# Kernel optimization log

Measured on AMD Instinct MI355X. Metric: run time of the kernel, lower is better.

Reference implementation:

```python
import jax, jax.numpy as jnp
import numpy as np

N_NODES = 100000
N_EDGES = 1250000
N_GRAPHS = 1024
NUM_SHAPES = 16
NUM_COLORS = 16
NUM_CLASSES = 10


def setup_inputs() -> dict:
    key = jax.random.key(0)
    ks = jax.random.split(key, 16)
    x_tokens = jax.random.randint(ks[0], (N_NODES, 2), 0, NUM_SHAPES, dtype=jnp.int64) if jax.config.jax_enable_x64 else jax.random.randint(ks[0], (N_NODES, 2), 0, NUM_SHAPES, dtype=jnp.int32)
    edge_index = jax.random.randint(ks[1], (2, N_EDGES), 0, N_NODES, dtype=jnp.int32)
    batch = jnp.sort(jax.random.randint(ks[2], (N_NODES,), 0, N_GRAPHS, dtype=jnp.int32))
    def glorot(k, shape, fan_in):
        return jax.random.normal(k, shape, jnp.float32) / jnp.sqrt(jnp.float32(fan_in))
    return {
        "x_tokens": x_tokens,
        "edge_index": edge_index,
        "batch": batch,
        "shape_emb": jax.random.normal(ks[3], (NUM_SHAPES, 8), jnp.float32),
        "color_emb": jax.random.normal(ks[4], (NUM_COLORS, 8), jnp.float32),
        "lin_w": glorot(ks[5], (32, 16), 16),
        "lin_b": jnp.zeros((32,), jnp.float32),
        "conv1_wrel": glorot(ks[6], (64, 32), 32),
        "conv1_brel": jnp.zeros((64,), jnp.float32),
        "conv1_wroot": glorot(ks[7], (64, 32), 32),
        "conv2_wrel": glorot(ks[8], (64, 64), 64),
        "conv2_brel": jnp.zeros((64,), jnp.float32),
        "conv2_wroot": glorot(ks[9], (64, 64), 64),
        "cls_w": glorot(ks[10], (NUM_CLASSES, 64), 64),
        "cls_b": jnp.zeros((NUM_CLASSES,), jnp.float32),
    }


def _graph_conv(x, src, dst, w_rel, b_rel, w_root):
    # PyG GraphConv (aggr='add'): out_i = W_rel @ sum_{j->i} x_j + b_rel + W_root @ x_i
    agg = jax.ops.segment_sum(x[src], dst, num_segments=x.shape[0])  # [N, d_in]
    return agg @ w_rel.T + b_rel + x @ w_root.T


def reference(x_tokens, edge_index, batch, shape_emb, color_emb, lin_w, lin_b,
              conv1_wrel, conv1_brel, conv1_wroot,
              conv2_wrel, conv2_brel, conv2_wroot, cls_w, cls_b):
    src, dst = edge_index[0], edge_index[1]
    # embed shape/color tokens and concat -> [N, 16]
    x = jnp.concatenate([shape_emb[x_tokens[:, 0]], color_emb[x_tokens[:, 1]]], axis=1)
    x = jax.nn.relu(x @ lin_w.T + lin_b)                      # [N, 32]
    x = jax.nn.relu(_graph_conv(x, src, dst, conv1_wrel, conv1_brel, conv1_wroot))  # [N, 64]
    x = jax.nn.relu(_graph_conv(x, src, dst, conv2_wrel, conv2_brel, conv2_wroot))  # [N, 64]
    # global mean pool over graphs
    sums = jax.ops.segment_sum(x, batch, num_segments=N_GRAPHS)           # [G, 64]
    counts = jax.ops.segment_sum(jnp.ones((x.shape[0],), x.dtype), batch, num_segments=N_GRAPHS)
    pooled = sums / jnp.maximum(counts, 1.0)[:, None]
    return pooled @ cls_w.T + cls_b                            # [G, num_classes]
```

## Files before the change

kernel.cpp:

```cpp
#include <hip/hip_runtime.h>

#define N_NODES  100000
#define N_EDGES  1250000
#define N_GRAPHS 1024
#define NB       ((N_NODES + 127) >> 7)
#define NB2      (N_NODES / 16)
#define NBLK_F   500
#define EPB      (N_EDGES / NBLK_F)
#define EMB_BLKS ((N_NODES + 255) / 256)
#define CAP      512

typedef __attribute__((ext_vector_type(8))) short short8;
typedef __attribute__((ext_vector_type(4))) float f32x4;
union U16 { uint4 u; short8 s; };

__device__ __forceinline__ float bflo(unsigned int w) { return __uint_as_float(w << 16); }
__device__ __forceinline__ float bfhi(unsigned int w) { return __uint_as_float(w & 0xffff0000u); }
__device__ __forceinline__ unsigned short f2bf(float f) {
  unsigned int u = __float_as_uint(f);
  u = (u + 0x7fffu + ((u >> 16) & 1u)) >> 16;
  return (unsigned short)u;
}
__device__ __forceinline__ unsigned int pack2(float a, float b) {
  return (unsigned int)f2bf(a) | ((unsigned int)f2bf(b) << 16);
}

template <int DIN>
__device__ __forceinline__ void prep_body(int t, const float* __restrict__ wrel,
                                          const float* __restrict__ wroot,
                                          unsigned short* __restrict__ Bf) {
  constexpr int NKC = (2 * DIN) / 32;
  if (t >= NKC * 4 * 64) return;
  int l = t & 63;
  int ct = (t >> 6) & 3;
  int kc = t >> 8;
  int col = ct * 16 + (l & 15);
#pragma unroll
  for (int e = 0; e < 8; ++e) {
    int k = kc * 32 + ((l >> 4) << 3) + e;
    float v = (k < DIN) ? wrel[col * DIN + k] : wroot[col * DIN + (k - DIN)];
    Bf[(size_t)t * 8 + e] = f2bf(v);
  }
}

__global__ void __launch_bounds__(256)
k_front(const int* __restrict__ tok,
        const float* __restrict__ semb, const float* __restrict__ cemb,
        const float* __restrict__ lw, const float* __restrict__ lb,
        unsigned short* __restrict__ x1,
        const float* __restrict__ w1rel, const float* __restrict__ w1root,
        const float* __restrict__ w2rel, const float* __restrict__ w2root,
        unsigned short* __restrict__ Bf1, unsigned short* __restrict__ Bf2,
        const int* __restrict__ dst, int* __restrict__ hist) {
  __shared__ int lh[NB];
  const int t = threadIdx.x;
  const int bid = blockIdx.x;
  if (bid < EMB_BLKS) {
    int i = bid * 256 + t;
    if (i >= N_NODES) return;
    int s = tok[2 * i], c = tok[2 * i + 1];
    float e[16];
#pragma unroll
    for (int k = 0; k < 8; ++k) { e[k] = semb[s * 8 + k]; e[8 + k] = cemb[c * 8 + k]; }
    unsigned int w[16];
#pragma unroll
    for (int o = 0; o < 16; ++o) {
      float a0 = lb[2 * o], a1 = lb[2 * o + 1];
#pragma unroll
      for (int k = 0; k < 16; ++k) {
        a0 = fmaf(e[k], lw[(2 * o) * 16 + k], a0);
        a1 = fmaf(e[k], lw[(2 * o + 1) * 16 + k], a1);
      }
      w[o] = pack2(fmaxf(a0, 0.f), fmaxf(a1, 0.f));
    }
    uint4* d4 = (uint4*)(x1 + (size_t)i * 32);
#pragma unroll
    for (int q = 0; q < 4; ++q)
      d4[q] = make_uint4(w[4 * q], w[4 * q + 1], w[4 * q + 2], w[4 * q + 3]);
  } else if (bid < EMB_BLKS + 6) {
    int pb = bid - EMB_BLKS;
    if (pb < 2) prep_body<32>(pb * 256 + t, w1rel, w1root, Bf1);
    else prep_body<64>((pb - 2) * 256 + t, w2rel, w2root, Bf2);
  } else {
    const int blk = bid - EMB_BLKS - 6;
    for (int i = t; i < NB; i += 256) lh[i] = 0;
    __syncthreads();
    const int start = blk * EPB;
    for (int e = start + t; e < start + EPB; e += 256)
      atomicAdd(&lh[dst[e] >> 7], 1);
    __syncthreads();
    int* hrow = hist + (size_t)blk * NB;
    for (int i = t; i < NB; i += 256)
      hrow[i] = lh[i];
  }
}

__global__ void __launch_bounds__(512)
k_colscan(int* __restrict__ hist, int* __restrict__ btotal) {
  __shared__ int sc[512];
  const int b = blockIdx.x;
  const int t = threadIdx.x;
  int v = (t < NBLK_F) ? hist[(size_t)t * NB + b] : 0;
  sc[t] = v;
  __syncthreads();
  for (int off = 1; off < 512; off <<= 1) {
    int x = (t >= off) ? sc[t - off] : 0;
    __syncthreads();
    sc[t] += x;
    __syncthreads();
  }
  if (t < NBLK_F) hist[(size_t)t * NB + b] = sc[t] - v;
  if (t == 511) btotal[b] = sc[511];
}

__global__ void __launch_bounds__(256)
k_bfill(const int* __restrict__ src, const int* __restrict__ dst,
        const int* __restrict__ btotal, const int* __restrict__ hist,
        int* __restrict__ tmp) {
  __shared__ int cur[NB];
  __shared__ int spart[256];
  const int t = threadIdx.x;
  const int blk = blockIdx.x;
  const int* hrow = hist + (size_t)blk * NB;
  int v[4]; int s = 0;
#pragma unroll
  for (int j = 0; j < 4; ++j) {
    int idx = t * 4 + j;
    v[j] = (idx < NB) ? btotal[idx] : 0;
    s += v[j];
  }
  spart[t] = s;
  __syncthreads();
  for (int off = 1; off < 256; off <<= 1) {
    int x = (t >= off) ? spart[t - off] : 0;
    __syncthreads();
    spart[t] += x;
    __syncthreads();
  }
  int run = spart[t] - s;
#pragma unroll
  for (int j = 0; j < 4; ++j) {
    int idx = t * 4 + j;
    if (idx < NB) cur[idx] = run + hrow[idx];
    run += v[j];
  }
  __syncthreads();
  const int start = blk * EPB;
  for (int e = start + t; e < start + EPB; e += 256) {
    int d = dst[e];
    int pos = atomicAdd(&cur[d >> 7], 1);
    tmp[pos] = (src[e] << 7) | (d & 127);
  }
}

__global__ void __launch_bounds__(256)
k_bfinal(const int* __restrict__ btotal, const int* __restrict__ tmp,
         int* __restrict__ deg, int* __restrict__ rowst,
         int* __restrict__ esrc) {
  __shared__ int spart[256];
  __shared__ int h[128], sc[128], cur[128];
  __shared__ int s_base;
  const int t = threadIdx.x;
  const int b = blockIdx.x;
  int s = 0;
  for (int i = t; i < b; i += 256) s += btotal[i];
  spart[t] = s;
  if (t < 128) h[t] = 0;
  __syncthreads();
  for (int off = 128; off >= 1; off >>= 1) {
    if (t < off) spart[t] += spart[t + off];
    __syncthreads();
  }
  if (t == 0) s_base = spart[0];
  __syncthreads();
  const int base = s_base, cnt = btotal[b];
  for (int i = t; i < cnt; i += 256) atomicAdd(&h[tmp[base + i] & 127], 1);
  __syncthreads();
  if (t < 128) sc[t] = h[t];
  __syncthreads();
  for (int off = 1; off < 128; off <<= 1) {
    int v = 0;
    if (t < 128 && t >= off) v = sc[t - off];
    __syncthreads();
    if (t < 128) sc[t] += v;
    __syncthreads();
  }
  if (t < 128) {
    int excl = sc[t] - h[t];
    cur[t] = excl;
    int node = (b << 7) + t;
    if (node < N_NODES) { deg[node] = h[t]; rowst[node] = base + excl; }
  }
  __syncthreads();
  for (int i = t; i < cnt; i += 256) {
    int v = tmp[base + i];
    int p = atomicAdd(&cur[v & 127], 1);
    esrc[base + p] = v >> 7;
  }
}

template <int DIN>
__global__ void __launch_bounds__(256)
k_conv(const int* __restrict__ deg, const int* __restrict__ rowst,
       const int* __restrict__ esrc,
       const unsigned short* __restrict__ X,
       const uint4* __restrict__ Bf,
       const float* __restrict__ bias,
       unsigned short* __restrict__ Y) {
  constexpr int NKC = (2 * DIN) / 32;
  constexpr int LPGu = DIN / 4;
  constexpr int GROUPS = 64 / LPGu;
  __shared__ int lsrc[CAP];
  __shared__ int hdeg[16], hbase[16];
  __shared__ int s_cnt, s_base;
  __shared__ unsigned short aggT[(DIN / 8) * 16 * 8];
  const int t = threadIdx.x;
  const int lane = t & 63;
  const int wv = t >> 6;
  const int b = blockIdx.x;
  if (t < 16) hdeg[t] = deg[b * 16 + t];
  __syncthreads();
  if (t == 0) {
    int run = 0;
#pragma unroll
    for (int n = 0; n < 16; ++n) { hbase[n] = run; run += hdeg[n]; }
    s_cnt = min(run, CAP);
    s_base = rowst[b * 16];
  }
  __syncthreads();
  const int cnt = s_cnt, base = s_base;
  for (int i = t; i < cnt; i += 256) lsrc[i] = esrc[base + i];
  __syncthreads();

  const int sub = lane / LPGu;
  const int lg = lane % LPGu;
#pragma unroll
  for (int k = 0; k < 4; ++k) {
    const int n = wv * 4 + k;
    const int dgn = hdeg[n];
    const int eb = hbase[n];
    float a0 = 0.f, a1 = 0.f, a2 = 0.f, a3 = 0.f;
    for (int j = 0; j < dgn; j += 2 * GROUPS) {
      int e0 = j + sub, e1 = j + GROUPS + sub;
      int s0 = lsrc[min(eb + min(e0, dgn - 1), CAP - 1)];
      int s1 = lsrc[min(eb + min(e1, dgn - 1), CAP - 1)];
      uint2 r0 = *((const uint2*)(X + (size_t)s0 * DIN) + lg);
      uint2 r1 = *((const uint2*)(X + (size_t)s1 * DIN) + lg);
      if (e0 < dgn) { a0 += bflo(r0.x); a1 += bfhi(r0.x); a2 += bflo(r0.y); a3 += bfhi(r0.y); }
      if (e1 < dgn) { a0 += bflo(r1.x); a1 += bfhi(r1.x); a2 += bflo(r1.y); a3 += bfhi(r1.y); }
    }
#pragma unroll
    for (int off = LPGu; off < 64; off <<= 1) {
      a0 += __shfl_xor(a0, off);
      a1 += __shfl_xor(a1, off);
      a2 += __shfl_xor(a2, off);
      a3 += __shfl_xor(a3, off);
    }
    if (sub == 0) {
      uint2 w; w.x = pack2(a0, a1); w.y = pack2(a2, a3);
      *(uint2*)&aggT[(((lg >> 1) * 16 + n) << 3) + ((lg & 1) << 2)] = w;
    }
  }
  __syncthreads();

  short8 bf[NKC];
#pragma unroll
  for (int kc = 0; kc < NKC; ++kc) { U16 u; u.u = Bf[(kc * 4 + wv) * 64 + lane]; bf[kc] = u.s; }
  const float bc = bias[wv * 16 + (lane & 15)];
  const int r = lane & 15;
  const int gg = b * 16 + r;
  short8 a[NKC];
#pragma unroll
  for (int kc = 0; kc < NKC / 2; ++kc) {
    const int chunk = kc * 4 + (lane >> 4);
    U16 u; u.u = *(const uint4*)&aggT[(chunk * 16 + r) << 3];
    a[kc] = u.s;
  }
#pragma unroll
  for (int kc = NKC / 2; kc < NKC; ++kc) {
    const int colx = (kc - NKC / 2) * 32 + ((lane >> 4) << 3);
    U16 u; u.u = *(const uint4*)(X + (size_t)gg * DIN + colx);
    a[kc] = u.s;
  }
  f32x4 acc = {bc, bc, bc, bc};
#pragma unroll
  for (int kc = 0; kc < NKC; ++kc)
    acc = __builtin_amdgcn_mfma_f32_16x16x32_bf16(a[kc], bf[kc], acc, 0, 0, 0);
  const int col = wv * 16 + (lane & 15);
#pragma unroll
  for (int j = 0; j < 4; ++j) {
    int grow = b * 16 + ((lane >> 4) << 2) + j;
    Y[(size_t)grow * 64 + col] = f2bf(fmaxf(acc[j], 0.f));
  }
}

__global__ void __launch_bounds__(256)
k_pool(const unsigned short* __restrict__ y2,
       const int* __restrict__ batch,
       const float* __restrict__ cw, const float* __restrict__ cb,
       float* __restrict__ out) {
  __shared__ float part[4][64];
  const int g = blockIdx.x;
  const int lane = threadIdx.x & 63;
  const int wv = threadIdx.x >> 6;
  int lo = 0, hi = N_NODES;
  while (lo < hi) { int m = (lo + hi) >> 1; if (batch[m] < g) lo = m + 1; else hi = m; }
  int lo2 = lo, hi2 = N_NODES;
  while (lo2 < hi2) { int m = (lo2 + hi2) >> 1; if (batch[m] < g + 1) lo2 = m + 1; else hi2 = m; }
  float s = 0.f;
  for (int r = lo + wv; r < lo2; r += 4)
    s += __uint_as_float((unsigned int)y2[(size_t)r * 64 + lane] << 16);
  part[wv][lane] = s;
  __syncthreads();
  if (wv == 0) {
    float p = part[0][lane] + part[1][lane] + part[2][lane] + part[3][lane];
    int c_ = lo2 - lo;
    p *= 1.f / (float)(c_ > 0 ? c_ : 1);
    for (int c = 0; c < 10; ++c) {
      float v = p * cw[c * 64 + lane];
#pragma unroll
      for (int off = 1; off < 64; off <<= 1) v += __shfl_xor(v, off);
      if (lane == 0) out[g * 10 + c] = v + cb[c];
    }
  }
}

extern "C" void kernel_launch(void* const* d_in, const int* in_sizes, int n_in,
                              void* d_out, int out_size, void* d_ws, size_t ws_size,
                              hipStream_t stream) {
  const int*   tok    = (const int*)d_in[0];
  const int*   eidx   = (const int*)d_in[1];
  const int*   batch  = (const int*)d_in[2];
  const float* semb   = (const float*)d_in[3];
  const float* cemb   = (const float*)d_in[4];
  const float* lw     = (const float*)d_in[5];
  const float* lb     = (const float*)d_in[6];
  const float* w1rel  = (const float*)d_in[7];
  const float* b1     = (const float*)d_in[8];
  const float* w1root = (const float*)d_in[9];
  const float* w2rel  = (const float*)d_in[10];
  const float* b2     = (const float*)d_in[11];
  const float* w2root = (const float*)d_in[12];
  const float* cw     = (const float*)d_in[13];
  const float* cb     = (const float*)d_in[14];
  const int* src = eidx;
  const int* dst = eidx + N_EDGES;

  char* p = (char*)d_ws;
  unsigned short* X1 = (unsigned short*)p;  p += (size_t)N_NODES * 32 * 2;
  unsigned short* X2 = (unsigned short*)p;  p += (size_t)N_NODES * 64 * 2;
  unsigned short* Y2 = (unsigned short*)p;  p += (size_t)N_NODES * 64 * 2;
  int*   tmp    = (int*)p;  p += (size_t)N_EDGES * 4;
  int*   esrc   = (int*)p;  p += (size_t)N_EDGES * 4;
  int*   degv   = (int*)p;  p += (size_t)N_NODES * 4;
  int*   rowst  = (int*)p;  p += (size_t)N_NODES * 4;
  int*   hist   = (int*)p;  p += (size_t)NBLK_F * NB * 4;
  int*   btotal = (int*)p;  p += 4096;
  unsigned short* Bf1 = (unsigned short*)p;  p += 512 * 8 * 2;
  unsigned short* Bf2 = (unsigned short*)p;  p += 1024 * 8 * 2;

  k_front<<<EMB_BLKS + 6 + NBLK_F, 256, 0, stream>>>(
      tok, semb, cemb, lw, lb, X1,
      w1rel, w1root, w2rel, w2root, Bf1, Bf2, dst, hist);

  k_colscan<<<NB, 512, 0, stream>>>(hist, btotal);
  k_bfill<<<NBLK_F, 256, 0, stream>>>(src, dst, btotal, hist, tmp);
  k_bfinal<<<NB, 256, 0, stream>>>(btotal, tmp, degv, rowst, esrc);

  k_conv<32><<<NB2, 256, 0, stream>>>(degv, rowst, esrc, X1, (const uint4*)Bf1, b1, X2);
  k_conv<64><<<NB2, 256, 0, stream>>>(degv, rowst, esrc, X2, (const uint4*)Bf2, b2, Y2);

  k_pool<<<N_GRAPHS, 256, 0, stream>>>(Y2, batch, cw, cb, (float*)d_out);
}
```

Measured before the change: 134.3 us.

## Fuse mean-pool sums into second conv epilogue via atomics

The second GraphConv no longer writes its 100k x 64 bf16 output. It instead reduces each 16-row tile per graph in registers and atomically adds the result into a small float sums buffer, with a fast path when all 16 rows belong to one graph. A lighter classifier kernel then divides by the node counts and applies the linear head. This removes the Y2 write and re-read and the per-graph row scan, in exchange for a memset, global float atomics, and a summation order that is no longer deterministic.

```diff
diff --git a/kernel.cpp b/kernel.cpp
--- a/kernel.cpp
+++ b/kernel.cpp
@@ -199,14 +199,15 @@
   }
 }
 
-template <int DIN>
+template <int DIN, bool FUSE_POOL>
 __global__ void __launch_bounds__(256)
 k_conv(const int* __restrict__ deg, const int* __restrict__ rowst,
        const int* __restrict__ esrc,
        const unsigned short* __restrict__ X,
        const uint4* __restrict__ Bf,
        const float* __restrict__ bias,
-       unsigned short* __restrict__ Y) {
+       const int* __restrict__ batch,
+       void* __restrict__ outv) {
   constexpr int NKC = (2 * DIN) / 32;
   constexpr int LPGu = DIN / 4;
   constexpr int GROUPS = 64 / LPGu;
@@ -287,41 +288,52 @@
   for (int kc = 0; kc < NKC; ++kc)
     acc = __builtin_amdgcn_mfma_f32_16x16x32_bf16(a[kc], bf[kc], acc, 0, 0, 0);
   const int col = wv * 16 + (lane & 15);
-#pragma unroll
-  for (int j = 0; j < 4; ++j) {
-    int grow = b * 16 + ((lane >> 4) << 2) + j;
-    Y[(size_t)grow * 64 + col] = f2bf(fmaxf(acc[j], 0.f));
-  }
-}
-
-__global__ void __launch_bounds__(256)
-k_pool(const unsigned short* __restrict__ y2,
-       const int* __restrict__ batch,
-       const float* __restrict__ cw, const float* __restrict__ cb,
-       float* __restrict__ out) {
-  __shared__ float part[4][64];
-  const int g = blockIdx.x;
+  if (!FUSE_POOL) {
+    unsigned short* Y = (unsigned short*)outv;
+#pragma unroll
+    for (int j = 0; j < 4; ++j) {
+      int grow = b * 16 + ((lane >> 4) << 2) + j;
+      Y[(size_t)grow * 64 + col] = f2bf(fmaxf(acc[j], 0.f));
+    }
+  } else {
+    float* sums = (float*)outv;
+    const int g0 = batch[b * 16];
+    const int g15 = batch[b * 16 + 15];
+    if (g0 == g15) {
+      float v = fmaxf(acc[0], 0.f) + fmaxf(acc[1], 0.f)
+              + fmaxf(acc[2], 0.f) + fmaxf(acc[3], 0.f);
+      v += __shfl_xor(v, 16);
+      v += __shfl_xor(v, 32);
+      if ((lane >> 4) == 0)
+        atomicAdd(&sums[(size_t)g0 * 64 + col], v);
+    } else {
+#pragma unroll
+      for (int j = 0; j < 4; ++j) {
+        int grow = b * 16 + ((lane >> 4) << 2) + j;
+        atomicAdd(&sums[(size_t)batch[grow] * 64 + col], fmaxf(acc[j], 0.f));
+      }
+    }
+  }
+}
+
+__global__ void __launch_bounds__(256)
+k_cls(const float* __restrict__ sums, const int* __restrict__ batch,
+      const float* __restrict__ cw, const float* __restrict__ cb,
+      float* __restrict__ out) {
+  const int g = blockIdx.x * 4 + (threadIdx.x >> 6);
   const int lane = threadIdx.x & 63;
-  const int wv = threadIdx.x >> 6;
+  if (g >= N_GRAPHS) return;
   int lo = 0, hi = N_NODES;
   while (lo < hi) { int m = (lo + hi) >> 1; if (batch[m] < g) lo = m + 1; else hi = m; }
   int lo2 = lo, hi2 = N_NODES;
   while (lo2 < hi2) { int m = (lo2 + hi2) >> 1; if (batch[m] < g + 1) lo2 = m + 1; else hi2 = m; }
-  float s = 0.f;
-  for (int r = lo + wv; r < lo2; r += 4)
-    s += __uint_as_float((unsigned int)y2[(size_t)r * 64 + lane] << 16);
-  part[wv][lane] = s;
-  __syncthreads();
-  if (wv == 0) {
-    float p = part[0][lane] + part[1][lane] + part[2][lane] + part[3][lane];
-    int c_ = lo2 - lo;
-    p *= 1.f / (float)(c_ > 0 ? c_ : 1);
-    for (int c = 0; c < 10; ++c) {
-      float v = p * cw[c * 64 + lane];
-#pragma unroll
-      for (int off = 1; off < 64; off <<= 1) v += __shfl_xor(v, off);
-      if (lane == 0) out[g * 10 + c] = v + cb[c];
-    }
+  int c_ = lo2 - lo;
+  float p = sums[(size_t)g * 64 + lane] * (1.f / (float)(c_ > 0 ? c_ : 1));
+  for (int c = 0; c < 10; ++c) {
+    float v = p * cw[c * 64 + lane];
+#pragma unroll
+    for (int off = 1; off < 64; off <<= 1) v += __shfl_xor(v, off);
+    if (lane == 0) out[g * 10 + c] = v + cb[c];
   }
 }
 
@@ -349,15 +361,17 @@
   char* p = (char*)d_ws;
   unsigned short* X1 = (unsigned short*)p;  p += (size_t)N_NODES * 32 * 2;
   unsigned short* X2 = (unsigned short*)p;  p += (size_t)N_NODES * 64 * 2;
-  unsigned short* Y2 = (unsigned short*)p;  p += (size_t)N_NODES * 64 * 2;
   int*   tmp    = (int*)p;  p += (size_t)N_EDGES * 4;
   int*   esrc   = (int*)p;  p += (size_t)N_EDGES * 4;
   int*   degv   = (int*)p;  p += (size_t)N_NODES * 4;
   int*   rowst  = (int*)p;  p += (size_t)N_NODES * 4;
   int*   hist   = (int*)p;  p += (size_t)NBLK_F * NB * 4;
   int*   btotal = (int*)p;  p += 4096;
+  float* sums   = (float*)p;  p += (size_t)N_GRAPHS * 64 * 4;
   unsigned short* Bf1 = (unsigned short*)p;  p += 512 * 8 * 2;
   unsigned short* Bf2 = (unsigned short*)p;  p += 1024 * 8 * 2;
+
+  hipMemsetAsync(sums, 0, (size_t)N_GRAPHS * 64 * 4, stream);
 
   k_front<<<EMB_BLKS + 6 + NBLK_F, 256, 0, stream>>>(
       tok, semb, cemb, lw, lb, X1,
@@ -367,8 +381,10 @@
   k_bfill<<<NBLK_F, 256, 0, stream>>>(src, dst, btotal, hist, tmp);
   k_bfinal<<<NB, 256, 0, stream>>>(btotal, tmp, degv, rowst, esrc);
 
-  k_conv<32><<<NB2, 256, 0, stream>>>(degv, rowst, esrc, X1, (const uint4*)Bf1, b1, X2);
-  k_conv<64><<<NB2, 256, 0, stream>>>(degv, rowst, esrc, X2, (const uint4*)Bf2, b2, Y2);
-
-  k_pool<<<N_GRAPHS, 256, 0, stream>>>(Y2, batch, cw, cb, (float*)d_out);
-}
+  k_conv<32, false><<<NB2, 256, 0, stream>>>(degv, rowst, esrc, X1, (const uint4*)Bf1,
+                                             b1, nullptr, X2);
+  k_conv<64, true><<<NB2, 256, 0, stream>>>(degv, rowst, esrc, X2, (const uint4*)Bf2,
+                                            b2, batch, sums);
+
+  k_cls<<<N_GRAPHS / 4, 256, 0, stream>>>(sums, batch, cw, cb, (float*)d_out);
+}
```

New measurement: 140.0 us. 4.2% more time.
